# Performance work log

Hardware: AMD Instinct MI355X
Metric: run time of the kernel (lower is better)

## Reference

```python
import jax, jax.numpy as jnp
import numpy as np

N = 20000      # nodes per snapshot
E = 320000     # directed edges per snapshot (self-loops added in reference)
T = 8          # snapshot sequence length
IN = 1         # in_dim
H = 32         # hidden_dim
HEADS = 2      # heads in first GAT layer
EPS = 1e-16    # PyG softmax denominator epsilon


def setup_inputs() -> dict:
    key = jax.random.key(0)
    ks = jax.random.split(key, 20)
    s = 0.1  # weight scale for numerical sanity
    return {
        "x": jax.random.normal(ks[0], (T, N, IN), jnp.float32),
        "edge_index": jax.random.randint(ks[1], (T, 2, E), 0, N, jnp.int64),
        # GAT layer 1: in=1 -> heads=2, out=32 (concat -> 64)
        "W1": jax.random.normal(ks[2], (IN, HEADS * H), jnp.float32) * s,
        "att_src1": jax.random.normal(ks[3], (HEADS, H), jnp.float32) * s,
        "att_dst1": jax.random.normal(ks[4], (HEADS, H), jnp.float32) * s,
        "b1": jax.random.normal(ks[5], (HEADS * H,), jnp.float32) * s,
        # GAT layer 2: in=64 -> heads=1, out=32
        "W2": jax.random.normal(ks[6], (HEADS * H, H), jnp.float32) * s,
        "att_src2": jax.random.normal(ks[7], (1, H), jnp.float32) * s,
        "att_dst2": jax.random.normal(ks[8], (1, H), jnp.float32) * s,
        "b2": jax.random.normal(ks[9], (H,), jnp.float32) * s,
        # GRU (torch layout: rows ordered r,z,n)
        "gru_w_ih": jax.random.normal(ks[10], (3 * H, H), jnp.float32) * s,
        "gru_w_hh": jax.random.normal(ks[11], (3 * H, H), jnp.float32) * s,
        "gru_b_ih": jax.random.normal(ks[12], (3 * H,), jnp.float32) * s,
        "gru_b_hh": jax.random.normal(ks[13], (3 * H,), jnp.float32) * s,
        # output head
        "fc_w": jax.random.normal(ks[14], (1, H), jnp.float32) * s,
        "fc_b": jax.random.normal(ks[15], (1,), jnp.float32) * s,
    }


def _gat_layer(x, src, dst, W, att_src, att_dst, bias, heads, dh):
    """PyG GATConv (shared src/dst lin, leaky_relu 0.2, per-dest softmax, concat heads)."""
    h = (x @ W).reshape(N, heads, dh)                      # [N,Hd,D]
    a_src = jnp.sum(h * att_src, axis=-1)                  # [N,Hd]
    a_dst = jnp.sum(h * att_dst, axis=-1)                  # [N,Hd]
    e = jax.nn.leaky_relu(a_src[src] + a_dst[dst], 0.2)    # [Eh,Hd]
    m = jax.ops.segment_max(e, dst, num_segments=N)        # per-dest max (stable)
    ex = jnp.exp(e - m[dst])
    denom = jax.ops.segment_sum(ex, dst, num_segments=N)
    alpha = ex / (denom[dst] + EPS)                        # [Eh,Hd]
    msg = h[src] * alpha[..., None]                        # [Eh,Hd,D]
    out = jax.ops.segment_sum(msg, dst, num_segments=N)    # [N,Hd,D]
    return out.reshape(N, heads * dh) + bias


def _encode(x_t, ei_t, W1, att_src1, att_dst1, b1, W2, att_src2, att_dst2, b2):
    loops = jnp.arange(N, dtype=ei_t.dtype)                # GATConv add_self_loops=True
    src = jnp.concatenate([ei_t[0], loops])
    dst = jnp.concatenate([ei_t[1], loops])
    h = jax.nn.elu(_gat_layer(x_t, src, dst, W1, att_src1, att_dst1, b1, HEADS, H))
    h = jax.nn.elu(_gat_layer(h, src, dst, W2, att_src2, att_dst2, b2, 1, H))
    return h                                                # [N,H]


def reference(x, edge_index, W1, att_src1, att_dst1, b1, W2, att_src2, att_dst2, b2,
              gru_w_ih, gru_w_hh, gru_b_ih, gru_b_hh, fc_w, fc_b):
    enc = jax.vmap(lambda xt, et: _encode(xt, et, W1, att_src1, att_dst1, b1,
                                          W2, att_src2, att_dst2, b2))(x, edge_index)  # [T,N,H]

    def gru_step(h, x_t):
        gi = x_t @ gru_w_ih.T + gru_b_ih                   # [N,3H]
        gh = h @ gru_w_hh.T + gru_b_hh
        ir, iz, in_ = jnp.split(gi, 3, axis=-1)
        hr, hz, hn = jnp.split(gh, 3, axis=-1)
        r = jax.nn.sigmoid(ir + hr)
        z = jax.nn.sigmoid(iz + hz)
        n = jnp.tanh(in_ + r * hn)
        h_new = (1.0 - z) * n + z * h
        return h_new, None

    h0 = jnp.zeros((N, H), enc.dtype)
    h_last, _ = jax.lax.scan(gru_step, h0, enc)            # last timestep hidden [N,H]
    pred = h_last @ fc_w.T + fc_b                          # [N,1]
    return pred
```

## Files before the change

kernel.cpp:

```cpp
#include <hip/hip_runtime.h>
#include <cmath>

#define NN 20000
#define NE 320000
#define TT 8
#define EPSF 1e-16f
#define NR 32
#define RSZ 625
#define NCH 1250

#define OFF_RT  0
#define OFF_ROW 1024
#define OFF_CSR (OFF_ROW + TT*(NN+1))
#define OFF_H2S (OFF_CSR + TT*NE/2)
#define OFF_AS2 (OFF_H2S + TT*NN*32)
#define OFF_AD2 (OFF_AS2 + TT*NN)
#define OFF_ENC (OFF_AD2 + TT*NN)
#define OFF_WP  (OFF_ENC + TT*NN*32)
#define WS_WORDS (OFF_WP + 6144)

__device__ __forceinline__ float fexp(float x) { return __expf(x); }
__device__ __forceinline__ float fsigmoid(float x) { return 1.f / (1.f + __expf(-x)); }
__device__ __forceinline__ float ftanh(float x) {
    float ax = fabsf(x);
    float e2 = __expf(-2.f * ax);
    float th = (1.f - e2) / (1.f + e2);
    return copysignf(th, x);
}

__global__ __launch_bounds__(256) void k_wpack(const float* __restrict__ wih,
                                               const float* __restrict__ whh,
                                               float* __restrict__ wp) {
    int i = blockIdx.x * 256 + threadIdx.x;
    if (i < 1024) {
        int k = i >> 5, j = i & 31;
        ((float4*)wp)[i] = make_float4(wih[j * 32 + k], wih[(32 + j) * 32 + k],
                                       wih[(64 + j) * 32 + k], whh[j * 32 + k]);
        ((float2*)(wp + 4096))[i] = make_float2(whh[(32 + j) * 32 + k],
                                                whh[(64 + j) * 32 + k]);
    }
}

__global__ __launch_bounds__(256) void k_bhist(const int* __restrict__ ei,
                                               int* __restrict__ bh) {
    int b = blockIdx.x;
    int t = b & 7, c = b >> 3;
    __shared__ int cnt[NR];
    int tid = threadIdx.x;
    if (tid < NR) cnt[tid] = 0;
    __syncthreads();
    int e = c * 256 + tid;
    int dst = ei[(size_t)t * 2 * NE + NE + e];
    int r = dst / RSZ;
    atomicAdd(&cnt[r], 1);
    __syncthreads();
    if (tid < NR) bh[(t * NCH + c) * NR + tid] = cnt[tid];
}

__global__ __launch_bounds__(256) void k_bscan1(int* __restrict__ bh,
                                                int* __restrict__ rt) {
    int b = blockIdx.x;
    int t = b & 7, r = b >> 3;
    __shared__ int sums[256];
    int tid = threadIdx.x;
    int c0 = tid * 5, c1 = c0 + 5; if (c1 > NCH) c1 = NCH; if (c0 > NCH) c0 = NCH;
    int v[5]; int s = 0;
    for (int c = c0, k = 0; c < c1; c++, k++) { v[k] = bh[(t * NCH + c) * NR + r]; s += v[k]; }
    sums[tid] = s;
    __syncthreads();
    if (tid == 0) {
        int acc = 0;
        for (int i = 0; i < 256; i++) { int x = sums[i]; sums[i] = acc; acc += x; }
        rt[t * NR + r] = acc;
    }
    __syncthreads();
    int acc = sums[tid];
    for (int c = c0, k = 0; c < c1; c++, k++) { bh[(t * NCH + c) * NR + r] = acc; acc += v[k]; }
}

__global__ __launch_bounds__(256) void k_bplace(const int* __restrict__ ei,
                                                const int* __restrict__ bh,
                                                const int* __restrict__ rt,
                                                unsigned* __restrict__ bkt) {
    int b = blockIdx.x;
    int t = b & 7, c = b >> 3;
    __shared__ int cnt[NR], base[NR], rbs[NR];
    int tid = threadIdx.x;
    if (tid == 0) {
        int acc = 0;
        for (int r = 0; r < NR; r++) { rbs[r] = acc; acc += rt[t * NR + r]; }
    }
    if (tid < NR) {
        cnt[tid] = 0;
        base[tid] = bh[(t * NCH + c) * NR + tid];
    }
    __syncthreads();
    int e = c * 256 + tid;
    int src = ei[(size_t)t * 2 * NE + e];
    int dst = ei[(size_t)t * 2 * NE + NE + e];
    int r = dst / RSZ;
    int pos = atomicAdd(&cnt[r], 1);
    bkt[(size_t)t * NE + rbs[r] + base[r] + pos] =
        ((unsigned)src << 10) | (unsigned)(dst - r * RSZ);
}

__global__ __launch_bounds__(256) void k_csr(const unsigned* __restrict__ bkt,
                                             const int* __restrict__ rt,
                                             int* __restrict__ row,
                                             unsigned short* __restrict__ csr) {
    int b = blockIdx.x;
    int t = b & 7, r = b >> 3;
    __shared__ int segs[2];
    __shared__ int deg[RSZ];
    __shared__ int cur[RSZ];
    __shared__ int sums[256];
    int tid = threadIdx.x;
    if (tid == 0) {
        int acc = 0, s0 = 0;
        for (int i = 0; i < NR; i++) { if (i == r) s0 = acc; acc += rt[t * NR + i]; }
        segs[0] = s0;
        segs[1] = (r == NR - 1) ? acc : s0 + rt[t * NR + r];
    }
    for (int i = tid; i < RSZ; i += 256) deg[i] = 0;
    __syncthreads();
    int seg0 = segs[0], seg1 = segs[1];
    int lo = r * RSZ;
    const unsigned* bp = bkt + (size_t)t * NE;
    for (int i = seg0 + tid; i < seg1; i += 256)
        atomicAdd(&deg[bp[i] & 1023], 1);
    __syncthreads();
    int c0 = tid * 3, c1 = c0 + 3; if (c1 > RSZ) c1 = RSZ; if (c0 > RSZ) c0 = RSZ;
    int v[3]; int s = 0;
    for (int i = c0, k = 0; i < c1; i++, k++) { v[k] = deg[i]; s += v[k]; }
    sums[tid] = s;
    __syncthreads();
    if (tid == 0) {
        int acc = 0;
        for (int i = 0; i < 256; i++) { int x = sums[i]; sums[i] = acc; acc += x; }
    }
    __syncthreads();
    int acc = sums[tid];
    for (int i = c0, k = 0; i < c1; i++, k++) {
        int off = seg0 + acc;
        row[t * (NN + 1) + lo + i] = off;
        cur[i] = off;
        acc += v[k];
    }
    if (r == NR - 1 && tid == 0) row[t * (NN + 1) + NN] = seg1;
    __syncthreads();
    unsigned short* cp = csr + (size_t)t * NE;
    for (int i = seg0 + tid; i < seg1; i += 256) {
        unsigned pk = bp[i];
        int pos = atomicAdd(&cur[pk & 1023], 1);
        cp[pos] = (unsigned short)(pk >> 10);
    }
}

__global__ __launch_bounds__(256) void k_l1(
        const float* __restrict__ x, const int* __restrict__ row,
        const unsigned short* __restrict__ csr,
        const float* __restrict__ as1, const float* __restrict__ ad1,
        const float* __restrict__ W1, const float* __restrict__ b1,
        const float* __restrict__ W2,
        const float* __restrict__ as2w, const float* __restrict__ ad2w,
        float* __restrict__ h2s, float* __restrict__ as2, float* __restrict__ ad2) {
    __shared__ float sW2[64 * 32];
    __shared__ float sW1[64], sb1[64], sas[32], sad[32], sc[4];
    int tid = threadIdx.x;
    for (int i = tid; i < 64 * 32; i += 256) sW2[i] = W2[i];
    if (tid < 64) { sW1[tid] = W1[tid]; sb1[tid] = b1[tid]; }
    if (tid < 32) { sas[tid] = as2w[tid]; sad[tid] = ad2w[tid]; }
    if (tid < 4) {
        int hd = tid & 1;
        const float* att = (tid < 2) ? as1 : ad1;
        float s = 0.f;
        for (int k = 0; k < 32; k++) s += W1[hd * 32 + k] * att[hd * 32 + k];
        sc[tid] = s;
    }
    __syncthreads();
    int b = blockIdx.x;
    int t = b & 7, chunk = b >> 3;
    int n = chunk * 256 + tid;
    if (n >= NN) return;
    int idx = t * NN + n;
    float cs0 = sc[0], cs1 = sc[1], cd0 = sc[2], cd1 = sc[3];
    float xd = x[idx];
    float v0 = xd * (cs0 + cd0); v0 = v0 > 0.f ? v0 : 0.2f * v0; float ex0 = fexp(v0);
    float v1 = xd * (cs1 + cd1); v1 = v1 > 0.f ? v1 : 0.2f * v1; float ex1 = fexp(v1);
    float den0 = ex0, den1 = ex1, S0 = ex0 * xd, S1 = ex1 * xd;
    int rs = row[t * (NN + 1) + n], re = row[t * (NN + 1) + n + 1];
    const unsigned short* cp = csr + (size_t)t * NE;
    const float* xp = x + t * NN;
    int i = rs;
    for (; i < re && (i & 3); i++) {
        int src = cp[i];
        float xs = xp[src];
        float u0 = xs * cs0 + xd * cd0; u0 = u0 > 0.f ? u0 : 0.2f * u0; float q0 = fexp(u0);
        float u1 = xs * cs1 + xd * cd1; u1 = u1 > 0.f ? u1 : 0.2f * u1; float q1 = fexp(u1);
        den0 += q0; S0 += q0 * xs;
        den1 += q1; S1 += q1 * xs;
    }
    for (; i + 4 <= re; i += 4) {
        ushort4 s4 = *(const ushort4*)(cp + i);
        float xA = xp[s4.x], xB = xp[s4.y], xC = xp[s4.z], xD = xp[s4.w];
        float uA0 = xA * cs0 + xd * cd0; uA0 = uA0 > 0.f ? uA0 : 0.2f * uA0; float qA0 = fexp(uA0);
        float uB0 = xB * cs0 + xd * cd0; uB0 = uB0 > 0.f ? uB0 : 0.2f * uB0; float qB0 = fexp(uB0);
        float uC0 = xC * cs0 + xd * cd0; uC0 = uC0 > 0.f ? uC0 : 0.2f * uC0; float qC0 = fexp(uC0);
        float uD0 = xD * cs0 + xd * cd0; uD0 = uD0 > 0.f ? uD0 : 0.2f * uD0; float qD0 = fexp(uD0);
        float uA1 = xA * cs1 + xd * cd1; uA1 = uA1 > 0.f ? uA1 : 0.2f * uA1; float qA1 = fexp(uA1);
        float uB1 = xB * cs1 + xd * cd1; uB1 = uB1 > 0.f ? uB1 : 0.2f * uB1; float qB1 = fexp(uB1);
        float uC1 = xC * cs1 + xd * cd1; uC1 = uC1 > 0.f ? uC1 : 0.2f * uC1; float qC1 = fexp(uC1);
        float uD1 = xD * cs1 + xd * cd1; uD1 = uD1 > 0.f ? uD1 : 0.2f * uD1; float qD1 = fexp(uD1);
        den0 += (qA0 + qB0) + (qC0 + qD0);
        S0 += qA0 * xA + qB0 * xB + qC0 * xC + qD0 * xD;
        den1 += (qA1 + qB1) + (qC1 + qD1);
        S1 += qA1 * xA + qB1 * xB + qC1 * xC + qD1 * xD;
    }
    for (; i < re; i++) {
        int src = cp[i];
        float xs = xp[src];
        float u0 = xs * cs0 + xd * cd0; u0 = u0 > 0.f ? u0 : 0.2f * u0; float q0 = fexp(u0);
        float u1 = xs * cs1 + xd * cd1; u1 = u1 > 0.f ? u1 : 0.2f * u1; float q1 = fexp(u1);
        den0 += q0; S0 += q0 * xs;
        den1 += q1; S1 += q1 * xs;
    }
    S0 /= (den0 + EPSF);
    S1 /= (den1 + EPSF);
    float h1[64];
#pragma unroll
    for (int d = 0; d < 64; d++) {
        float v = sW1[d] * (d < 32 ? S0 : S1) + sb1[d];
        h1[d] = v > 0.f ? v : fexp(v) - 1.f;
    }
    float4 acc4[8];
#pragma unroll
    for (int q = 0; q < 8; q++) acc4[q] = make_float4(0.f, 0.f, 0.f, 0.f);
    const float4* w4 = (const float4*)sW2;
#pragma unroll 8
    for (int d = 0; d < 64; d++) {
        float hd = h1[d];
#pragma unroll
        for (int q = 0; q < 8; q++) {
            float4 w = w4[d * 8 + q];
            acc4[q].x += hd * w.x; acc4[q].y += hd * w.y;
            acc4[q].z += hd * w.z; acc4[q].w += hd * w.w;
        }
    }
    float a_s = 0.f, a_d = 0.f;
    float4* op = (float4*)(h2s + (size_t)idx * 32);
#pragma unroll
    for (int q = 0; q < 8; q++) {
        float4 a = acc4[q];
        op[q] = a;
        a_s += a.x * sas[4 * q] + a.y * sas[4 * q + 1] + a.z * sas[4 * q + 2] + a.w * sas[4 * q + 3];
        a_d += a.x * sad[4 * q] + a.y * sad[4 * q + 1] + a.z * sad[4 * q + 2] + a.w * sad[4 * q + 3];
    }
    as2[idx] = a_s;
    ad2[idx] = a_d;
}

__global__ __launch_bounds__(256) void k_l2(
        const int* __restrict__ row, const unsigned short* __restrict__ csr,
        const float* __restrict__ as2, const float* __restrict__ ad2,
        const float* __restrict__ h2s, const float* __restrict__ b2,
        float* __restrict__ enc) {
    int tid = threadIdx.x;
    int g = tid >> 5, lane = tid & 31;
    int b = blockIdx.x;
    int t = b & 7, chunk = b >> 3;
    int n = chunk * 8 + g;
    int pair = t * NN + n;
    int base = t * NN;
    const float* hb = h2s + (size_t)base * 32;
    float adn = ad2[pair];
    float vs = as2[pair] + adn; vs = vs > 0.f ? vs : 0.2f * vs;
    float qs = fexp(vs);
    float num = qs * hb[(size_t)n * 32 + lane];
    float den_part = 0.f;
    int rs = row[t * (NN + 1) + n], re = row[t * (NN + 1) + n + 1];
    const unsigned short* cp = csr + (size_t)t * NE;
    for (int i0 = rs; i0 < re; i0 += 32) {
        int cnt = re - i0; if (cnt > 32) cnt = 32;
        float q = 0.f; int s = 0;
        if (lane < cnt) {
            s = cp[i0 + lane];
            float a = as2[base + s];
            float u = a + adn; u = u > 0.f ? u : 0.2f * u;
            q = fexp(u);
        }
        den_part += q;
        int e = 0;
        for (; e + 2 <= cnt; e += 2) {
            float q0 = __shfl(q, e, 32);
            int   s0 = __shfl(s, e, 32);
            float q1 = __shfl(q, e + 1, 32);
            int   s1 = __shfl(s, e + 1, 32);
            num += q0 * hb[(size_t)s0 * 32 + lane];
            num += q1 * hb[(size_t)s1 * 32 + lane];
        }
        if (e < cnt) {
            float q0 = __shfl(q, e, 32);
            int   s0 = __shfl(s, e, 32);
            num += q0 * hb[(size_t)s0 * 32 + lane];
        }
    }
    float den = den_part;
#pragma unroll
    for (int off = 16; off > 0; off >>= 1) den += __shfl_xor(den, off, 32);
    den += qs;
    float ev = num / (den + EPSF) + b2[lane];
    ev = ev > 0.f ? ev : fexp(ev) - 1.f;
    enc[(size_t)pair * 32 + lane] = ev;
}

__global__ __launch_bounds__(128) void k_gru(
        const float* __restrict__ enc, const float* __restrict__ wp,
        const float* __restrict__ bih, const float* __restrict__ bhh,
        const float* __restrict__ fcw, const float* __restrict__ fcb,
        float* __restrict__ out) {
    __shared__ float4 wpA[32 * 32];
    __shared__ float2 wpB[32 * 32];
    __shared__ float sbih[96], sbhh[96], sfw[32];
    __shared__ float4 e4[4][32], h4[4][32];
    int tid = threadIdx.x;
    const float4* wpAg = (const float4*)wp;
    const float2* wpBg = (const float2*)(wp + 4096);
    for (int i = tid; i < 1024; i += 128) { wpA[i] = wpAg[i]; wpB[i] = wpBg[i]; }
    if (tid < 96) { sbih[tid] = bih[tid]; sbhh[tid] = bhh[tid]; }
    if (tid < 32) sfw[tid] = fcw[tid];
    int g = tid >> 5, lane = tid & 31;
    int n0 = blockIdx.x * 16 + g * 4;
    float h0 = 0.f, h1 = 0.f, h2 = 0.f, h3 = 0.f;
    h4[g][lane] = make_float4(0.f, 0.f, 0.f, 0.f);
    __syncthreads();
    float bi_r = sbih[lane], bi_z = sbih[32 + lane], bi_n = sbih[64 + lane];
    float bh_r = sbhh[lane], bh_z = sbhh[32 + lane], bh_n = sbhh[64 + lane];
    const float* ep0 = enc + (size_t)n0 * 32 + lane;
    float4 ecur = make_float4(ep0[0], ep0[32], ep0[64], ep0[96]);
    for (int t = 0; t < TT; t++) {
        e4[g][lane] = ecur;
        __builtin_amdgcn_wave_barrier();
        if (t < TT - 1) {
            const float* ep = enc + ((size_t)((t + 1) * NN + n0)) * 32 + lane;
            ecur = make_float4(ep[0], ep[32], ep[64], ep[96]);
        }
        float ir0 = bi_r, ir1 = bi_r, ir2 = bi_r, ir3 = bi_r;
        float iz0 = bi_z, iz1 = bi_z, iz2 = bi_z, iz3 = bi_z;
        float in0 = bi_n, in1 = bi_n, in2 = bi_n, in3 = bi_n;
        float hr0 = bh_r, hr1 = bh_r, hr2 = bh_r, hr3 = bh_r;
        float hz0 = bh_z, hz1 = bh_z, hz2 = bh_z, hz3 = bh_z;
        float hn0 = bh_n, hn1 = bh_n, hn2 = bh_n, hn3 = bh_n;
#pragma unroll 16
        for (int k = 0; k < 32; k++) {
            float4 wa = wpA[k * 32 + lane];
            float2 wb = wpB[k * 32 + lane];
            float4 ek = e4[g][k];
            float4 hk = h4[g][k];
            ir0 += wa.x * ek.x; ir1 += wa.x * ek.y; ir2 += wa.x * ek.z; ir3 += wa.x * ek.w;
            iz0 += wa.y * ek.x; iz1 += wa.y * ek.y; iz2 += wa.y * ek.z; iz3 += wa.y * ek.w;
            in0 += wa.z * ek.x; in1 += wa.z * ek.y; in2 += wa.z * ek.z; in3 += wa.z * ek.w;
            hr0 += wa.w * hk.x; hr1 += wa.w * hk.y; hr2 += wa.w * hk.z; hr3 += wa.w * hk.w;
            hz0 += wb.x * hk.x; hz1 += wb.x * hk.y; hz2 += wb.x * hk.z; hz3 += wb.x * hk.w;
            hn0 += wb.y * hk.x; hn1 += wb.y * hk.y; hn2 += wb.y * hk.z; hn3 += wb.y * hk.w;
        }
        __builtin_amdgcn_wave_barrier();
        {
            float r, z, nn_;
            r = fsigmoid(ir0 + hr0); z = fsigmoid(iz0 + hz0);
            nn_ = ftanh(in0 + r * hn0); h0 = (1.f - z) * nn_ + z * h0;
            r = fsigmoid(ir1 + hr1); z = fsigmoid(iz1 + hz1);
            nn_ = ftanh(in1 + r * hn1); h1 = (1.f - z) * nn_ + z * h1;
            r = fsigmoid(ir2 + hr2); z = fsigmoid(iz2 + hz2);
            nn_ = ftanh(in2 + r * hn2); h2 = (1.f - z) * nn_ + z * h2;
            r = fsigmoid(ir3 + hr3); z = fsigmoid(iz3 + hz3);
            nn_ = ftanh(in3 + r * hn3); h3 = (1.f - z) * nn_ + z * h3;
        }
        h4[g][lane] = make_float4(h0, h1, h2, h3);
        __builtin_amdgcn_wave_barrier();
    }
    float fw = sfw[lane], fb = fcb[0];
    float v0 = h0 * fw, v1 = h1 * fw, v2 = h2 * fw, v3 = h3 * fw;
#pragma unroll
    for (int off = 16; off > 0; off >>= 1) {
        v0 += __shfl_down(v0, off, 32);
        v1 += __shfl_down(v1, off, 32);
        v2 += __shfl_down(v2, off, 32);
        v3 += __shfl_down(v3, off, 32);
    }
    if (lane == 0) {
        out[n0 + 0] = v0 + fb;
        out[n0 + 1] = v1 + fb;
        out[n0 + 2] = v2 + fb;
        out[n0 + 3] = v3 + fb;
    }
}

extern "C" void kernel_launch(void* const* d_in, const int* in_sizes, int n_in,
                              void* d_out, int out_size, void* d_ws, size_t ws_size,
                              hipStream_t stream) {
    const float* x    = (const float*)d_in[0];
    const int*   ei   = (const int*)d_in[1];
    const float* W1   = (const float*)d_in[2];
    const float* as1  = (const float*)d_in[3];
    const float* ad1  = (const float*)d_in[4];
    const float* b1   = (const float*)d_in[5];
    const float* W2   = (const float*)d_in[6];
    const float* as2w = (const float*)d_in[7];
    const float* ad2w = (const float*)d_in[8];
    const float* b2   = (const float*)d_in[9];
    const float* wih  = (const float*)d_in[10];
    const float* whh  = (const float*)d_in[11];
    const float* bih  = (const float*)d_in[12];
    const float* bhh  = (const float*)d_in[13];
    const float* fcw  = (const float*)d_in[14];
    const float* fcb  = (const float*)d_in[15];
    float* ws  = (float*)d_ws;
    float* out = (float*)d_out;

    int*            rt   = (int*)(ws + OFF_RT);
    int*            rowp = (int*)(ws + OFF_ROW);
    unsigned short* csr  = (unsigned short*)(ws + OFF_CSR);
    int*            bh   = (int*)(ws + OFF_H2S);
    unsigned*       bkt  = (unsigned*)(ws + OFF_ENC);
    float*          wp   = ws + OFF_WP;

    k_wpack<<<4, 256, 0, stream>>>(wih, whh, wp);
    k_bhist<<<TT * NCH, 256, 0, stream>>>(ei, bh);
    k_bscan1<<<TT * NR, 256, 0, stream>>>(bh, rt);
    k_bplace<<<TT * NCH, 256, 0, stream>>>(ei, bh, rt, bkt);
    k_csr<<<TT * NR, 256, 0, stream>>>(bkt, rt, rowp, csr);

    k_l1<<<TT * ((NN + 255) / 256), 256, 0, stream>>>(x, rowp, csr, as1, ad1,
                                              W1, b1, W2, as2w, ad2w,
                                              ws + OFF_H2S, ws + OFF_AS2, ws + OFF_AD2);

    k_l2<<<TT * (NN / 8), 256, 0, stream>>>(rowp, csr, ws + OFF_AS2, ws + OFF_AD2,
                                            ws + OFF_H2S, b2, ws + OFF_ENC);

    k_gru<<<NN / 16, 128, 0, stream>>>(ws + OFF_ENC, wp, bih, bhh,
                                       fcw, fcb, out);
}
```

Baseline: 283.0 us.

## Fuse CSR build with GAT layer-1 using shared-memory atomic aggregation over finer buckets

Splits nodes into 80 buckets of 250 instead of 32 of 625, and merges the CSR construction kernel with the first GAT layer. Layer-1 softmax sums are now built by shared-memory float atomics while streaming the bucketed edges, so the separate pass that re-reads the CSR and gathers x is gone, along with one kernel launch. The CSR and row offsets are still written for layer 2. The cost is heavy LDS atomic contention, only 250 of 256 threads active in the dense phase, and a summation order that depends on atomic timing. The bucket tile is packed with 8 bits, which requires src << 8 to fit.

New measurement: 326.8 us. 1.15x slower.

```diff
diff --git a/kernel.cpp b/kernel.cpp
--- a/kernel.cpp
+++ b/kernel.cpp
@@ -5,8 +5,8 @@
 #define NE 320000
 #define TT 8
 #define EPSF 1e-16f
-#define NR 32
-#define RSZ 625
+#define NRR 80
+#define RSZ 250
 #define NCH 1250
 
 #define OFF_RT  0
@@ -45,16 +45,16 @@
                                                int* __restrict__ bh) {
     int b = blockIdx.x;
     int t = b & 7, c = b >> 3;
-    __shared__ int cnt[NR];
-    int tid = threadIdx.x;
-    if (tid < NR) cnt[tid] = 0;
+    __shared__ int cnt[NRR];
+    int tid = threadIdx.x;
+    if (tid < NRR) cnt[tid] = 0;
     __syncthreads();
     int e = c * 256 + tid;
     int dst = ei[(size_t)t * 2 * NE + NE + e];
     int r = dst / RSZ;
     atomicAdd(&cnt[r], 1);
     __syncthreads();
-    if (tid < NR) bh[(t * NCH + c) * NR + tid] = cnt[tid];
+    if (tid < NRR) bh[(t * NCH + c) * NRR + tid] = cnt[tid];
 }
 
 __global__ __launch_bounds__(256) void k_bscan1(int* __restrict__ bh,
@@ -65,17 +65,17 @@
     int tid = threadIdx.x;
     int c0 = tid * 5, c1 = c0 + 5; if (c1 > NCH) c1 = NCH; if (c0 > NCH) c0 = NCH;
     int v[5]; int s = 0;
-    for (int c = c0, k = 0; c < c1; c++, k++) { v[k] = bh[(t * NCH + c) * NR + r]; s += v[k]; }
+    for (int c = c0, k = 0; c < c1; c++, k++) { v[k] = bh[(t * NCH + c) * NRR + r]; s += v[k]; }
     sums[tid] = s;
     __syncthreads();
     if (tid == 0) {
         int acc = 0;
         for (int i = 0; i < 256; i++) { int x = sums[i]; sums[i] = acc; acc += x; }
-        rt[t * NR + r] = acc;
+        rt[t * NRR + r] = acc;
     }
     __syncthreads();
     int acc = sums[tid];
-    for (int c = c0, k = 0; c < c1; c++, k++) { bh[(t * NCH + c) * NR + r] = acc; acc += v[k]; }
+    for (int c = c0, k = 0; c < c1; c++, k++) { bh[(t * NCH + c) * NRR + r] = acc; acc += v[k]; }
 }
 
 __global__ __launch_bounds__(256) void k_bplace(const int* __restrict__ ei,
@@ -84,15 +84,15 @@
                                                 unsigned* __restrict__ bkt) {
     int b = blockIdx.x;
     int t = b & 7, c = b >> 3;
-    __shared__ int cnt[NR], base[NR], rbs[NR];
+    __shared__ int cnt[NRR], base[NRR], rbs[NRR];
     int tid = threadIdx.x;
     if (tid == 0) {
         int acc = 0;
-        for (int r = 0; r < NR; r++) { rbs[r] = acc; acc += rt[t * NR + r]; }
-    }
-    if (tid < NR) {
+        for (int r = 0; r < NRR; r++) { rbs[r] = acc; acc += rt[t * NRR + r]; }
+    }
+    if (tid < NRR) {
         cnt[tid] = 0;
-        base[tid] = bh[(t * NCH + c) * NR + tid];
+        base[tid] = bh[(t * NCH + c) * NRR + tid];
     }
     __syncthreads();
     int e = c * 256 + tid;
@@ -101,73 +101,27 @@
     int r = dst / RSZ;
     int pos = atomicAdd(&cnt[r], 1);
     bkt[(size_t)t * NE + rbs[r] + base[r] + pos] =
-        ((unsigned)src << 10) | (unsigned)(dst - r * RSZ);
-}
-
-__global__ __launch_bounds__(256) void k_csr(const unsigned* __restrict__ bkt,
-                                             const int* __restrict__ rt,
-                                             int* __restrict__ row,
-                                             unsigned short* __restrict__ csr) {
-    int b = blockIdx.x;
-    int t = b & 7, r = b >> 3;
-    __shared__ int segs[2];
-    __shared__ int deg[RSZ];
-    __shared__ int cur[RSZ];
-    __shared__ int sums[256];
-    int tid = threadIdx.x;
-    if (tid == 0) {
-        int acc = 0, s0 = 0;
-        for (int i = 0; i < NR; i++) { if (i == r) s0 = acc; acc += rt[t * NR + i]; }
-        segs[0] = s0;
-        segs[1] = (r == NR - 1) ? acc : s0 + rt[t * NR + r];
-    }
-    for (int i = tid; i < RSZ; i += 256) deg[i] = 0;
-    __syncthreads();
-    int seg0 = segs[0], seg1 = segs[1];
-    int lo = r * RSZ;
-    const unsigned* bp = bkt + (size_t)t * NE;
-    for (int i = seg0 + tid; i < seg1; i += 256)
-        atomicAdd(&deg[bp[i] & 1023], 1);
-    __syncthreads();
-    int c0 = tid * 3, c1 = c0 + 3; if (c1 > RSZ) c1 = RSZ; if (c0 > RSZ) c0 = RSZ;
-    int v[3]; int s = 0;
-    for (int i = c0, k = 0; i < c1; i++, k++) { v[k] = deg[i]; s += v[k]; }
-    sums[tid] = s;
-    __syncthreads();
-    if (tid == 0) {
-        int acc = 0;
-        for (int i = 0; i < 256; i++) { int x = sums[i]; sums[i] = acc; acc += x; }
-    }
-    __syncthreads();
-    int acc = sums[tid];
-    for (int i = c0, k = 0; i < c1; i++, k++) {
-        int off = seg0 + acc;
-        row[t * (NN + 1) + lo + i] = off;
-        cur[i] = off;
-        acc += v[k];
-    }
-    if (r == NR - 1 && tid == 0) row[t * (NN + 1) + NN] = seg1;
-    __syncthreads();
-    unsigned short* cp = csr + (size_t)t * NE;
-    for (int i = seg0 + tid; i < seg1; i += 256) {
-        unsigned pk = bp[i];
-        int pos = atomicAdd(&cur[pk & 1023], 1);
-        cp[pos] = (unsigned short)(pk >> 10);
-    }
-}
-
-__global__ __launch_bounds__(256) void k_l1(
-        const float* __restrict__ x, const int* __restrict__ row,
-        const unsigned short* __restrict__ csr,
+        ((unsigned)src << 8) | (unsigned)(dst - r * RSZ);
+}
+
+__global__ __launch_bounds__(256) void k_csr_l1(
+        const unsigned* __restrict__ bkt, const int* __restrict__ rt,
+        const float* __restrict__ x,
         const float* __restrict__ as1, const float* __restrict__ ad1,
         const float* __restrict__ W1, const float* __restrict__ b1,
         const float* __restrict__ W2,
         const float* __restrict__ as2w, const float* __restrict__ ad2w,
+        int* __restrict__ row, unsigned short* __restrict__ csr,
         float* __restrict__ h2s, float* __restrict__ as2, float* __restrict__ ad2) {
-    __shared__ float sW2[64 * 32];
+    int b = blockIdx.x;
+    int t = b & 7, r = b >> 3;
+    __shared__ float sW2[2048];
     __shared__ float sW1[64], sb1[64], sas[32], sad[32], sc[4];
-    int tid = threadIdx.x;
-    for (int i = tid; i < 64 * 32; i += 256) sW2[i] = W2[i];
+    __shared__ float xl[RSZ];
+    __shared__ float den0[RSZ], den1[RSZ], S0a[RSZ], S1a[RSZ];
+    __shared__ int deg[RSZ], cur[RSZ], sums[256], segs[2];
+    int tid = threadIdx.x;
+    for (int i = tid; i < 2048; i += 256) sW2[i] = W2[i];
     if (tid < 64) { sW1[tid] = W1[tid]; sb1[tid] = b1[tid]; }
     if (tid < 32) { sas[tid] = as2w[tid]; sad[tid] = ad2w[tid]; }
     if (tid < 4) {
@@ -177,86 +131,104 @@
         for (int k = 0; k < 32; k++) s += W1[hd * 32 + k] * att[hd * 32 + k];
         sc[tid] = s;
     }
-    __syncthreads();
-    int b = blockIdx.x;
-    int t = b & 7, chunk = b >> 3;
-    int n = chunk * 256 + tid;
-    if (n >= NN) return;
-    int idx = t * NN + n;
+    if (tid == 0) {
+        int acc = 0, s0 = 0;
+        for (int i = 0; i < NRR; i++) { if (i == r) s0 = acc; acc += rt[t * NRR + i]; }
+        segs[0] = s0;
+        segs[1] = (r == NRR - 1) ? acc : s0 + rt[t * NRR + r];
+    }
+    int lo = r * RSZ;
+    if (tid < RSZ) {
+        xl[tid] = x[t * NN + lo + tid];
+        den0[tid] = 0.f; den1[tid] = 0.f; S0a[tid] = 0.f; S1a[tid] = 0.f;
+        deg[tid] = 0;
+    }
+    __syncthreads();
+    int seg0 = segs[0], seg1 = segs[1];
     float cs0 = sc[0], cs1 = sc[1], cd0 = sc[2], cd1 = sc[3];
-    float xd = x[idx];
-    float v0 = xd * (cs0 + cd0); v0 = v0 > 0.f ? v0 : 0.2f * v0; float ex0 = fexp(v0);
-    float v1 = xd * (cs1 + cd1); v1 = v1 > 0.f ? v1 : 0.2f * v1; float ex1 = fexp(v1);
-    float den0 = ex0, den1 = ex1, S0 = ex0 * xd, S1 = ex1 * xd;
-    int rs = row[t * (NN + 1) + n], re = row[t * (NN + 1) + n + 1];
-    const unsigned short* cp = csr + (size_t)t * NE;
-    const float* xp = x + t * NN;
-    int i = rs;
-    for (; i < re && (i & 3); i++) {
-        int src = cp[i];
-        float xs = xp[src];
-        float u0 = xs * cs0 + xd * cd0; u0 = u0 > 0.f ? u0 : 0.2f * u0; float q0 = fexp(u0);
-        float u1 = xs * cs1 + xd * cd1; u1 = u1 > 0.f ? u1 : 0.2f * u1; float q1 = fexp(u1);
-        den0 += q0; S0 += q0 * xs;
-        den1 += q1; S1 += q1 * xs;
-    }
-    for (; i + 4 <= re; i += 4) {
-        ushort4 s4 = *(const ushort4*)(cp + i);
-        float xA = xp[s4.x], xB = xp[s4.y], xC = xp[s4.z], xD = xp[s4.w];
-        float uA0 = xA * cs0 + xd * cd0; uA0 = uA0 > 0.f ? uA0 : 0.2f * uA0; float qA0 = fexp(uA0);
-        float uB0 = xB * cs0 + xd * cd0; uB0 = uB0 > 0.f ? uB0 : 0.2f * uB0; float qB0 = fexp(uB0);
-        float uC0 = xC * cs0 + xd * cd0; uC0 = uC0 > 0.f ? uC0 : 0.2f * uC0; float qC0 = fexp(uC0);
-        float uD0 = xD * cs0 + xd * cd0; uD0 = uD0 > 0.f ? uD0 : 0.2f * uD0; float qD0 = fexp(uD0);
-        float uA1 = xA * cs1 + xd * cd1; uA1 = uA1 > 0.f ? uA1 : 0.2f * uA1; float qA1 = fexp(uA1);
-        float uB1 = xB * cs1 + xd * cd1; uB1 = uB1 > 0.f ? uB1 : 0.2f * uB1; float qB1 = fexp(uB1);
-        float uC1 = xC * cs1 + xd * cd1; uC1 = uC1 > 0.f ? uC1 : 0.2f * uC1; float qC1 = fexp(uC1);
-        float uD1 = xD * cs1 + xd * cd1; uD1 = uD1 > 0.f ? uD1 : 0.2f * uD1; float qD1 = fexp(uD1);
-        den0 += (qA0 + qB0) + (qC0 + qD0);
-        S0 += qA0 * xA + qB0 * xB + qC0 * xC + qD0 * xD;
-        den1 += (qA1 + qB1) + (qC1 + qD1);
-        S1 += qA1 * xA + qB1 * xB + qC1 * xC + qD1 * xD;
-    }
-    for (; i < re; i++) {
-        int src = cp[i];
-        float xs = xp[src];
-        float u0 = xs * cs0 + xd * cd0; u0 = u0 > 0.f ? u0 : 0.2f * u0; float q0 = fexp(u0);
-        float u1 = xs * cs1 + xd * cd1; u1 = u1 > 0.f ? u1 : 0.2f * u1; float q1 = fexp(u1);
-        den0 += q0; S0 += q0 * xs;
-        den1 += q1; S1 += q1 * xs;
-    }
-    S0 /= (den0 + EPSF);
-    S1 /= (den1 + EPSF);
-    float h1[64];
-#pragma unroll
-    for (int d = 0; d < 64; d++) {
-        float v = sW1[d] * (d < 32 ? S0 : S1) + sb1[d];
-        h1[d] = v > 0.f ? v : fexp(v) - 1.f;
-    }
-    float4 acc4[8];
-#pragma unroll
-    for (int q = 0; q < 8; q++) acc4[q] = make_float4(0.f, 0.f, 0.f, 0.f);
-    const float4* w4 = (const float4*)sW2;
+    const unsigned* bp = bkt + (size_t)t * NE;
+    const float* xg = x + t * NN;
+    for (int i = seg0 + tid; i < seg1; i += 512) {
+        unsigned pkA = bp[i];
+        int iB = i + 256;
+        unsigned pkB = (iB < seg1) ? bp[iB] : 0u;
+        int dlA = pkA & 255, sA = pkA >> 8;
+        float xsA = xg[sA], xdA = xl[dlA];
+        atomicAdd(&deg[dlA], 1);
+        float u0 = xsA * cs0 + xdA * cd0; u0 = u0 > 0.f ? u0 : 0.2f * u0; float q0 = fexp(u0);
+        float u1 = xsA * cs1 + xdA * cd1; u1 = u1 > 0.f ? u1 : 0.2f * u1; float q1 = fexp(u1);
+        atomicAdd(&den0[dlA], q0); atomicAdd(&S0a[dlA], q0 * xsA);
+        atomicAdd(&den1[dlA], q1); atomicAdd(&S1a[dlA], q1 * xsA);
+        if (iB < seg1) {
+            int dlB = pkB & 255, sB = pkB >> 8;
+            float xsB = xg[sB], xdB = xl[dlB];
+            atomicAdd(&deg[dlB], 1);
+            float w0 = xsB * cs0 + xdB * cd0; w0 = w0 > 0.f ? w0 : 0.2f * w0; float p0 = fexp(w0);
+            float w1 = xsB * cs1 + xdB * cd1; w1 = w1 > 0.f ? w1 : 0.2f * w1; float p1 = fexp(w1);
+            atomicAdd(&den0[dlB], p0); atomicAdd(&S0a[dlB], p0 * xsB);
+            atomicAdd(&den1[dlB], p1); atomicAdd(&S1a[dlB], p1 * xsB);
+        }
+    }
+    __syncthreads();
+    sums[tid] = (tid < RSZ) ? deg[tid] : 0;
+    __syncthreads();
+    if (tid == 0) {
+        int acc = 0;
+        for (int i = 0; i < 256; i++) { int v = sums[i]; sums[i] = acc; acc += v; }
+    }
+    __syncthreads();
+    if (tid < RSZ) {
+        int off = seg0 + sums[tid];
+        row[t * (NN + 1) + lo + tid] = off;
+        cur[tid] = off;
+    }
+    if (r == NRR - 1 && tid == 0) row[t * (NN + 1) + NN] = seg1;
+    __syncthreads();
+    unsigned short* cp = csr + (size_t)t * NE;
+    for (int i = seg0 + tid; i < seg1; i += 256) {
+        unsigned pk = bp[i];
+        int pos = atomicAdd(&cur[pk & 255], 1);
+        cp[pos] = (unsigned short)(pk >> 8);
+    }
+    if (tid < RSZ) {
+        int idx = t * NN + lo + tid;
+        float xd = xl[tid];
+        float v0 = xd * (cs0 + cd0); v0 = v0 > 0.f ? v0 : 0.2f * v0; float ex0 = fexp(v0);
+        float v1 = xd * (cs1 + cd1); v1 = v1 > 0.f ? v1 : 0.2f * v1; float ex1 = fexp(v1);
+        float Sv0 = (S0a[tid] + ex0 * xd) / (den0[tid] + ex0 + EPSF);
+        float Sv1 = (S1a[tid] + ex1 * xd) / (den1[tid] + ex1 + EPSF);
+        float h1[64];
+#pragma unroll
+        for (int d = 0; d < 64; d++) {
+            float v = sW1[d] * (d < 32 ? Sv0 : Sv1) + sb1[d];
+            h1[d] = v > 0.f ? v : fexp(v) - 1.f;
+        }
+        float4 acc4[8];
+#pragma unroll
+        for (int q = 0; q < 8; q++) acc4[q] = make_float4(0.f, 0.f, 0.f, 0.f);
+        const float4* w4 = (const float4*)sW2;
 #pragma unroll 8
-    for (int d = 0; d < 64; d++) {
-        float hd = h1[d];
+        for (int d = 0; d < 64; d++) {
+            float hd = h1[d];
+#pragma unroll
+            for (int q = 0; q < 8; q++) {
+                float4 w = w4[d * 8 + q];
+                acc4[q].x += hd * w.x; acc4[q].y += hd * w.y;
+                acc4[q].z += hd * w.z; acc4[q].w += hd * w.w;
+            }
+        }
+        float a_s = 0.f, a_d = 0.f;
+        float4* op = (float4*)(h2s + (size_t)idx * 32);
 #pragma unroll
         for (int q = 0; q < 8; q++) {
-            float4 w = w4[d * 8 + q];
-            acc4[q].x += hd * w.x; acc4[q].y += hd * w.y;
-            acc4[q].z += hd * w.z; acc4[q].w += hd * w.w;
-        }
-    }
-    float a_s = 0.f, a_d = 0.f;
-    float4* op = (float4*)(h2s + (size_t)idx * 32);
-#pragma unroll
-    for (int q = 0; q < 8; q++) {
-        float4 a = acc4[q];
-        op[q] = a;
-        a_s += a.x * sas[4 * q] + a.y * sas[4 * q + 1] + a.z * sas[4 * q + 2] + a.w * sas[4 * q + 3];
-        a_d += a.x * sad[4 * q] + a.y * sad[4 * q + 1] + a.z * sad[4 * q + 2] + a.w * sad[4 * q + 3];
-    }
-    as2[idx] = a_s;
-    ad2[idx] = a_d;
+            float4 a = acc4[q];
+            op[q] = a;
+            a_s += a.x * sas[4 * q] + a.y * sas[4 * q + 1] + a.z * sas[4 * q + 2] + a.w * sas[4 * q + 3];
+            a_d += a.x * sad[4 * q] + a.y * sad[4 * q + 1] + a.z * sad[4 * q + 2] + a.w * sad[4 * q + 3];
+        }
+        as2[idx] = a_s;
+        ad2[idx] = a_d;
+    }
 }
 
 __global__ __launch_bounds__(256) void k_l2(
@@ -426,13 +398,11 @@
 
     k_wpack<<<4, 256, 0, stream>>>(wih, whh, wp);
     k_bhist<<<TT * NCH, 256, 0, stream>>>(ei, bh);
-    k_bscan1<<<TT * NR, 256, 0, stream>>>(bh, rt);
+    k_bscan1<<<TT * NRR, 256, 0, stream>>>(bh, rt);
     k_bplace<<<TT * NCH, 256, 0, stream>>>(ei, bh, rt, bkt);
-    k_csr<<<TT * NR, 256, 0, stream>>>(bkt, rt, rowp, csr);
-
-    k_l1<<<TT * ((NN + 255) / 256), 256, 0, stream>>>(x, rowp, csr, as1, ad1,
-                                              W1, b1, W2, as2w, ad2w,
-                                              ws + OFF_H2S, ws + OFF_AS2, ws + OFF_AD2);
+    k_csr_l1<<<TT * NRR, 256, 0, stream>>>(bkt, rt, x, as1, ad1, W1, b1, W2,
+                                           as2w, ad2w, rowp, csr,
+                                           ws + OFF_H2S, ws + OFF_AS2, ws + OFF_AD2);
 
     k_l2<<<TT * (NN / 8), 256, 0, stream>>>(rowp, csr, ws + OFF_AS2, ws + OFF_AD2,
                                             ws + OFF_H2S, b2, ws + OFF_ENC);
```
